# Kernel tuning notes

Hardware: AMD Instinct MI355X
Metric: run time of the kernel (lower is better)

Reference implementation:

```python
import jax, jax.numpy as jnp
import numpy as np

X_DIM, Y_DIM = 16, 8
D_MODEL, N_HEADS, N_LAYERS = 256, 8, 8
D_HEAD = D_MODEL // N_HEADS            # 32 (hidden_out_size // n_heads)
D_FF = D_HEAD * 8 * N_HEADS            # 2048 (feed_forward_dimensions)
B, S_PAST, S_FUT = 4, 1024, 512
MIN_STD = 0.01
LN_EPS = 1e-5
ATTN_EPS = 1e-6


def setup_inputs() -> dict:
    key = jax.random.key(0)
    ks = jax.random.split(key, 24)
    def nrm(k, shape, s=0.02):
        return jax.random.normal(k, shape, jnp.float32) * s
    L, d, dff = N_LAYERS, D_MODEL, D_FF
    x_size = X_DIM + Y_DIM
    return {
        "past_x": jax.random.normal(ks[0], (B, S_PAST, X_DIM), jnp.float32),
        "past_y": jax.random.normal(ks[1], (B, S_PAST, Y_DIM), jnp.float32),
        "future_x": jax.random.normal(ks[2], (B, S_FUT, X_DIM), jnp.float32),
        "enc_W": nrm(ks[3], (x_size, d)), "enc_b": jnp.zeros((d,), jnp.float32),
        "Wq": nrm(ks[4], (L, d, d)), "bq": jnp.zeros((L, d), jnp.float32),
        "Wk": nrm(ks[5], (L, d, d)), "bk": jnp.zeros((L, d), jnp.float32),
        "Wv": nrm(ks[6], (L, d, d)), "bv": jnp.zeros((L, d), jnp.float32),
        "Wo": nrm(ks[7], (L, d, d)), "bo": jnp.zeros((L, d), jnp.float32),
        "ln1_w": jnp.ones((L, d), jnp.float32), "ln1_b": jnp.zeros((L, d), jnp.float32),
        "W1": nrm(ks[8], (L, d, dff)), "b1": jnp.zeros((L, dff), jnp.float32),
        "W2": nrm(ks[9], (L, dff, d)), "b2": jnp.zeros((L, d), jnp.float32),
        "ln2_w": jnp.ones((L, d), jnp.float32), "ln2_b": jnp.zeros((L, d), jnp.float32),
        "mean_W": nrm(ks[10], (d, Y_DIM)), "mean_b": jnp.zeros((Y_DIM,), jnp.float32),
        "std_W": nrm(ks[11], (d, Y_DIM)), "std_b": jnp.zeros((Y_DIM,), jnp.float32),
    }


def _ln(x, w, b):
    m = jnp.mean(x, axis=-1, keepdims=True)
    v = jnp.var(x, axis=-1, keepdims=True)
    return (x - m) * jax.lax.rsqrt(v + LN_EPS) * w + b


def _causal_linear_attn(q, k, v):
    # q,k,v: [B, N, H, D]; phi(x) = elu(x) + 1 (fast_transformers default feature map)
    q = jax.nn.elu(q) + 1.0
    k = jax.nn.elu(k) + 1.0
    # cumulative outer-product state S_i = sum_{j<=i} phi(k_j) v_j^T : [B,N,H,D,D]
    kv = jnp.cumsum(jnp.einsum('bnhd,bnhm->bnhdm', k, v), axis=1)
    num = jnp.einsum('bnhd,bnhdm->bnhm', q, kv)
    z = jnp.einsum('bnhd,bnhd->bnh', q, jnp.cumsum(k, axis=1))
    return num / (z[..., None] + ATTN_EPS)


def _forward(past_x, past_y, future_x, enc_W, enc_b, Wq, bq, Wk, bk, Wv, bv,
             Wo, bo, ln1_w, ln1_b, W1, b1, W2, b2, ln2_w, ln2_b,
             mean_W, mean_b, std_W, std_b):
    Bz, Sf = future_x.shape[0], future_x.shape[1]
    steps = past_y.shape[1]
    # future y placeholder = last observed y, repeated
    fy = jnp.repeat(past_y[:, -1:, :], Sf, axis=1)
    context = jnp.concatenate([past_x, past_y], axis=-1)
    target = jnp.concatenate([future_x, fy], axis=-1)
    x = jax.lax.stop_gradient(jnp.concatenate([context, target], axis=1))  # .detach()
    x = x @ enc_W + enc_b                      # [B, N, D_MODEL]
    N = x.shape[1]
    for i in range(N_LAYERS):
        q = (x @ Wq[i] + bq[i]).reshape(Bz, N, N_HEADS, D_HEAD)
        k = (x @ Wk[i] + bk[i]).reshape(Bz, N, N_HEADS, D_HEAD)
        v = (x @ Wv[i] + bv[i]).reshape(Bz, N, N_HEADS, D_HEAD)
        a = _causal_linear_attn(q, k, v).reshape(Bz, N, D_MODEL)
        x = _ln(x + (a @ Wo[i] + bo[i]), ln1_w[i], ln1_b[i])   # post-norm (fast_transformers)
        y = jax.nn.relu(x @ W1[i] + b1[i]) @ W2[i] + b2[i]
        x = _ln(x + y, ln2_w[i], ln2_b[i])
    out = x[:, steps:, :]                      # keep only the target segment
    mean = out @ mean_W + mean_b
    sigma = MIN_STD + (1.0 - MIN_STD) * jax.nn.softplus(out @ std_W + std_b)
    return mean, sigma


def reference(past_x, past_y, future_x, enc_W, enc_b, Wq, bq, Wk, bk, Wv, bv,
              Wo, bo, ln1_w, ln1_b, W1, b1, W2, b2, ln2_w, ln2_b,
              mean_W, mean_b, std_W, std_b):
    return _forward(past_x, past_y, future_x, enc_W, enc_b, Wq, bq, Wk, bk,
                    Wv, bv, Wo, bo, ln1_w, ln1_b, W1, b1, W2, b2,
                    ln2_w, ln2_b, mean_W, mean_b, std_W, std_b)
```

## Files before the change

### kernel.cpp

```cpp
#include <hip/hip_runtime.h>
#include <hip/hip_bf16.h>
#include <math.h>

#define BB 4
#define SP 1024
#define SF 512
#define NN 1536
#define DD 256
#define HH 8
#define DH 32
#define DFF 2048
#define LL 8
#define TOK (BB*NN)
#define FTOK (BB*SF)
#define NSEG 48
#define SEGLEN 32

typedef __attribute__((ext_vector_type(8))) short bf16x8;
typedef __attribute__((ext_vector_type(4))) float f32x4;
typedef __hip_bfloat16 bf16;

__device__ __forceinline__ void gld_lds16(const void* g, void* l) {
    __builtin_amdgcn_global_load_lds(
        (const __attribute__((address_space(1))) void*)g,
        (__attribute__((address_space(3))) void*)l, 16, 0, 0);
}

__device__ __forceinline__ unsigned short f2bf_u(float f) {
    return __builtin_bit_cast(unsigned short, __float2bfloat16(f));
}

__device__ __forceinline__ int futmap(int f) {
    return (f >> 9)*NN + SP + (f & 511);
}

__device__ __forceinline__ void wtrans_tile(
    const float* __restrict__ s, bf16* __restrict__ d, int K, int N,
    int k0, int n0)
{
    __shared__ float tile[64][65];
    int t = threadIdx.x, c = t & 63, r4 = t >> 6;
    #pragma unroll
    for (int rr = 0; rr < 64; rr += 4)
        tile[rr+r4][c] = s[(size_t)(k0+rr+r4)*N + n0 + c];
    __syncthreads();
    #pragma unroll
    for (int rr = 0; rr < 64; rr += 4) {
        int n = rr + r4;
        d[(size_t)(n0+n)*K + k0 + c] = __float2bfloat16(tile[c][n]);
    }
}

__global__ __launch_bounds__(256) void wtrans_kernel(
    const float* __restrict__ src, bf16* __restrict__ dst, int K, int N)
{
    wtrans_tile(src + (size_t)blockIdx.z*K*N, dst + (size_t)blockIdx.z*K*N,
                K, N, blockIdx.x*64, blockIdx.y*64);
}

__global__ __launch_bounds__(256) void wtrans4_kernel(
    const float* __restrict__ Wq, const float* __restrict__ Wk,
    const float* __restrict__ Wv, const float* __restrict__ Wo,
    bf16* __restrict__ Wqt, bf16* __restrict__ Wkt,
    bf16* __restrict__ Wvt, bf16* __restrict__ Wot)
{
    int z = blockIdx.z, which = z >> 3, l = z & 7;
    const float* s = (which == 0 ? Wq : which == 1 ? Wk : which == 2 ? Wv : Wo)
                     + (size_t)l*DD*DD;
    bf16* d = (which == 0 ? Wqt : which == 1 ? Wkt : which == 2 ? Wvt : Wot)
              + (size_t)l*DD*DD;
    wtrans_tile(s, d, DD, DD, blockIdx.x*64, blockIdx.y*64);
}

template<int BM, bool BOUT>
__device__ __forceinline__ void gemm_core(
    const bf16* __restrict__ A, const bf16* __restrict__ Wt,
    const float* __restrict__ bias, float* __restrict__ Cf,
    bf16* __restrict__ Cb, int N, int K, int epi, int kc0, int kc1, int fut)
{
    constexpr int MI = BM/32;
    __shared__ bf16 As[BM*64];
    __shared__ bf16 Bs[128*64];
    int tid = threadIdx.x, lane = tid & 63, wid = tid >> 6;
    int m0 = blockIdx.x*BM, n0 = blockIdx.y*128;
    if (fut) m0 = futmap(m0);
    int wm = (wid & 1)*(BM/2), wn = (wid >> 1)*64;

    f32x4 acc[MI][4] = {};

    int rA = wid*(BM/4) + (lane >> 3);
    int rB = wid*32 + (lane >> 3);
    int c_st = (lane & 7)*8;
    const bf16* Ag = A  + (size_t)(m0 + rA)*K + c_st;
    const bf16* Bg = Wt + (size_t)(n0 + rB)*K + c_st;
    bf16* Asw = As + (wid*(BM/4))*64;
    bf16* Bsw = Bs + (wid*32)*64;

    int a_off = (wm + (lane & 15))*64 + (lane >> 4)*8;
    int b_off = (wn + (lane & 15))*64 + (lane >> 4)*8;

    for (int kc = kc0; kc < kc1; kc += 64) {
        #pragma unroll
        for (int i = 0; i < MI; i++)
            gld_lds16(Ag + (size_t)(i*8)*K + kc, Asw + (i*8)*64);
        #pragma unroll
        for (int i = 0; i < 4; i++)
            gld_lds16(Bg + (size_t)(i*8)*K + kc, Bsw + (i*8)*64);
        __syncthreads();
        #pragma unroll
        for (int ks = 0; ks < 2; ks++) {
            bf16x8 af[MI], bfr[4];
            #pragma unroll
            for (int i = 0; i < MI; i++)
                af[i] = *(const bf16x8*)(As + a_off + i*16*64 + ks*32);
            #pragma unroll
            for (int j = 0; j < 4; j++)
                bfr[j] = *(const bf16x8*)(Bs + b_off + j*16*64 + ks*32);
            #pragma unroll
            for (int i = 0; i < MI; i++)
                #pragma unroll
                for (int j = 0; j < 4; j++)
                    acc[i][j] = __builtin_amdgcn_mfma_f32_16x16x32_bf16(
                        af[i], bfr[j], acc[i][j], 0, 0, 0);
        }
        __syncthreads();
    }

    if constexpr (BOUT) {
        bf16* Ct = Bs;
        #pragma unroll
        for (int j = 0; j < 4; j++) {
            int col = wn + j*16 + (lane & 15);
            float bv = bias[n0 + col];
            #pragma unroll
            for (int i = 0; i < MI; i++) {
                #pragma unroll
                for (int r = 0; r < 4; r++) {
                    int row = wm + i*16 + (lane >> 4)*4 + r;
                    float v = acc[i][j][r] + bv;
                    if (epi == 1) v = fmaxf(v, 0.f);
                    else if (epi == 2) v = (v > 0.f) ? v + 1.f : expf(v);
                    Ct[row*128 + (col ^ (((row >> 2) & 3) << 4))] = __float2bfloat16(v);
                }
            }
        }
        __syncthreads();
        constexpr int NU = BM/16;
        #pragma unroll
        for (int u = 0; u < NU; u++) {
            int e = (u*256 + tid)*8;
            int row = e >> 7, c0 = e & 127;
            bf16x8 val = *(const bf16x8*)(Ct + row*128 + (c0 ^ (((row >> 2) & 3) << 4)));
            *(bf16x8*)(Cb + (size_t)(m0 + row)*N + n0 + c0) = val;
        }
    } else {
        int col_base = n0 + wn + (lane & 15);
        int row_base = m0 + wm + (lane >> 4)*4;
        #pragma unroll
        for (int j = 0; j < 4; j++) {
            int col = col_base + j*16;
            float bv = bias[col];
            #pragma unroll
            for (int i = 0; i < MI; i++) {
                #pragma unroll
                for (int r = 0; r < 4; r++) {
                    int row = row_base + i*16 + r;
                    float v = acc[i][j][r] + bv;
                    if (epi == 1) v = fmaxf(v, 0.f);
                    else if (epi == 2) v = (v > 0.f) ? v + 1.f : expf(v);
                    if (Cb) Cb[(size_t)row*N + col] = __float2bfloat16(v);
                    else    Cf[(size_t)row*N + col] = v;
                }
            }
        }
    }
}

template<int BM, bool BOUT>
__global__ __launch_bounds__(256) void mfma_gemm_kernel(
    const bf16* __restrict__ A, const bf16* __restrict__ Wt,
    const float* __restrict__ bias, float* __restrict__ Cf,
    bf16* __restrict__ Cb, int N, int K, int epi, int fut)
{
    gemm_core<BM, BOUT>(A, Wt, bias, Cf, Cb, N, K, epi, 0, K, fut);
}

template<int BM>
__global__ __launch_bounds__(256) void mfma_qkv_kernel(
    const bf16* __restrict__ Xb,
    const bf16* __restrict__ Wqt, const bf16* __restrict__ Wkt, const bf16* __restrict__ Wvt,
    const float* __restrict__ bq, const float* __restrict__ bk, const float* __restrict__ bv,
    float* __restrict__ Q, float* __restrict__ K, float* __restrict__ V, int layer)
{
    int z = blockIdx.z;
    const bf16* Wt = (z == 0) ? Wqt : (z == 1) ? Wkt : Wvt;
    const float* b = (z == 0) ? bq : (z == 1) ? bk : bv;
    float* C = (z == 0) ? Q : (z == 1) ? K : V;
    gemm_core<BM, false>(Xb, Wt + (size_t)layer*DD*DD, b + (size_t)layer*DD,
                         C, nullptr, DD, DD, (z == 2) ? 0 : 2, 0, DD, 0);
}

__global__ __launch_bounds__(256) void w2_slice_kernel(
    const bf16* __restrict__ A, const bf16* __restrict__ Wt,
    float* __restrict__ G4, int fut)
{
    __shared__ bf16 As[32*64];
    __shared__ bf16 Bs[256*64];
    int tid = threadIdx.x, lane = tid & 63, wid = tid >> 6;
    int m0 = blockIdx.x*32;
    if (fut) m0 = futmap(m0);
    int z = blockIdx.y;
    int kc0 = z*(DFF/4), kc1 = kc0 + DFF/4;
    int wn = wid*64;

    f32x4 acc[2][4] = {};

    int rA = wid*8 + (lane >> 3);
    int c_st = (lane & 7)*8;
    const bf16* Ag = A + (size_t)(m0 + rA)*DFF + c_st;
    const bf16* Bg = Wt + (size_t)(wn + (lane >> 3))*DFF + c_st;
    bf16* Asw = As + (wid*8)*64;
    bf16* Bsw = Bs + wn*64;

    int a_off = (lane & 15)*64 + (lane >> 4)*8;
    int b_off = (wn + (lane & 15))*64 + (lane >> 4)*8;

    for (int kc = kc0; kc < kc1; kc += 64) {
        gld_lds16(Ag + kc, Asw);
        #pragma unroll
        for (int i = 0; i < 8; i++)
            gld_lds16(Bg + (size_t)(i*8)*DFF + kc, Bsw + (i*8)*64);
        __syncthreads();
        #pragma unroll
        for (int ks = 0; ks < 2; ks++) {
            bf16x8 af[2], bfr[4];
            af[0] = *(const bf16x8*)(As + a_off + ks*32);
            af[1] = *(const bf16x8*)(As + a_off + 16*64 + ks*32);
            #pragma unroll
            for (int j = 0; j < 4; j++)
                bfr[j] = *(const bf16x8*)(Bs + b_off + j*16*64 + ks*32);
            #pragma unroll
            for (int i = 0; i < 2; i++)
                #pragma unroll
                for (int j = 0; j < 4; j++)
                    acc[i][j] = __builtin_amdgcn_mfma_f32_16x16x32_bf16(
                        af[i], bfr[j], acc[i][j], 0, 0, 0);
        }
        __syncthreads();
    }

    float* Gz = G4 + (size_t)z*TOK*DD;
    #pragma unroll
    for (int j = 0; j < 4; j++) {
        int c = wn + j*16 + (lane & 15);
        #pragma unroll
        for (int i = 0; i < 2; i++) {
            int row = m0 + i*16 + (lane >> 4)*4;
            #pragma unroll
            for (int r = 0; r < 4; r++)
                Gz[(size_t)(row + r)*DD + c] = acc[i][j][r];
        }
    }
}

__global__ __launch_bounds__(256) void wo_ln_kernel(
    const bf16* __restrict__ A, const bf16* __restrict__ Wt,
    const float* __restrict__ bias,
    const float* __restrict__ lnw, const float* __restrict__ lnb,
    float* __restrict__ X, bf16* __restrict__ Xb, int fut)
{
    __shared__ bf16 As[32*64];
    __shared__ bf16 Bs[256*64];
    __shared__ float red[2][4][32];
    int tid = threadIdx.x, lane = tid & 63, wid = tid >> 6;
    int m0 = blockIdx.x*32;
    if (fut) m0 = futmap(m0);
    int wn = wid*64;

    f32x4 acc[2][4] = {};

    int rA = wid*8 + (lane >> 3);
    int c_st = (lane & 7)*8;
    const bf16* Ag = A + (size_t)(m0 + rA)*DD + c_st;
    const bf16* Bg = Wt + (size_t)(wn + (lane >> 3))*DD + c_st;
    bf16* Asw = As + (wid*8)*64;
    bf16* Bsw = Bs + wn*64;

    int a_off = (lane & 15)*64 + (lane >> 4)*8;
    int b_off = (wn + (lane & 15))*64 + (lane >> 4)*8;

    for (int kc = 0; kc < DD; kc += 64) {
        gld_lds16(Ag + kc, Asw);
        #pragma unroll
        for (int i = 0; i < 8; i++)
            gld_lds16(Bg + (size_t)(i*8)*DD + kc, Bsw + (i*8)*64);
        __syncthreads();
        #pragma unroll
        for (int ks = 0; ks < 2; ks++) {
            bf16x8 af[2], bfr[4];
            af[0] = *(const bf16x8*)(As + a_off + ks*32);
            af[1] = *(const bf16x8*)(As + a_off + 16*64 + ks*32);
            #pragma unroll
            for (int j = 0; j < 4; j++)
                bfr[j] = *(const bf16x8*)(Bs + b_off + j*16*64 + ks*32);
            #pragma unroll
            for (int i = 0; i < 2; i++)
                #pragma unroll
                for (int j = 0; j < 4; j++)
                    acc[i][j] = __builtin_amdgcn_mfma_f32_16x16x32_bf16(
                        af[i], bfr[j], acc[i][j], 0, 0, 0);
        }
        __syncthreads();
    }

    #pragma unroll
    for (int j = 0; j < 4; j++) {
        int c = wn + j*16 + (lane & 15);
        float bv = bias[c];
        #pragma unroll
        for (int i = 0; i < 2; i++) {
            int row = m0 + i*16 + (lane >> 4)*4;
            #pragma unroll
            for (int r = 0; r < 4; r++)
                acc[i][j][r] += bv + X[(size_t)(row + r)*DD + c];
        }
    }
    #pragma unroll
    for (int i = 0; i < 2; i++) {
        #pragma unroll
        for (int r = 0; r < 4; r++) {
            float s  = (acc[i][0][r] + acc[i][1][r]) + (acc[i][2][r] + acc[i][3][r]);
            float s2 = (acc[i][0][r]*acc[i][0][r] + acc[i][1][r]*acc[i][1][r])
                     + (acc[i][2][r]*acc[i][2][r] + acc[i][3][r]*acc[i][3][r]);
            #pragma unroll
            for (int off = 1; off < 16; off <<= 1) {
                s  += __shfl_xor(s,  off, 64);
                s2 += __shfl_xor(s2, off, 64);
            }
            if ((lane & 15) == 0) {
                int rloc = i*16 + (lane >> 4)*4 + r;
                red[0][wid][rloc] = s;
                red[1][wid][rloc] = s2;
            }
        }
    }
    __syncthreads();
    #pragma unroll
    for (int i = 0; i < 2; i++) {
        #pragma unroll
        for (int r = 0; r < 4; r++) {
            int rloc = i*16 + (lane >> 4)*4 + r;
            float S  = (red[0][0][rloc] + red[0][1][rloc]) + (red[0][2][rloc] + red[0][3][rloc]);
            float S2 = (red[1][0][rloc] + red[1][1][rloc]) + (red[1][2][rloc] + red[1][3][rloc]);
            float mean = S * (1.f/256.f);
            float var  = S2 * (1.f/256.f) - mean*mean;
            float rs = rsqrtf(var + 1e-5f);
            #pragma unroll
            for (int j = 0; j < 4; j++) {
                int c = wn + j*16 + (lane & 15);
                float o = (acc[i][j][r] - mean) * rs * lnw[c] + lnb[c];
                size_t idx = (size_t)(m0 + rloc)*DD + c;
                X[idx] = o;
                Xb[idx] = __float2bfloat16(o);
            }
        }
    }
}

__global__ __launch_bounds__(256) void encode_kernel(
    const float* __restrict__ px, const float* __restrict__ py,
    const float* __restrict__ fx, const float* __restrict__ encW,
    const float* __restrict__ encb, float* __restrict__ X, bf16* __restrict__ Xb)
{
    int tok = blockIdx.x;
    int t = threadIdx.x;
    int b = tok / NN, n = tok % NN;
    __shared__ float in[24];
    if (t < 16) {
        in[t] = (n < SP) ? px[((size_t)b*SP + n)*16 + t]
                         : fx[((size_t)b*SF + (n - SP))*16 + t];
    } else if (t < 24) {
        int j = t - 16;
        in[t] = (n < SP) ? py[((size_t)b*SP + n)*8 + j]
                         : py[((size_t)b*SP + (SP-1))*8 + j];
    }
    __syncthreads();
    float acc = encb[t];
    #pragma unroll
    for (int j = 0; j < 24; j++) acc = fmaf(in[j], encW[j*DD + t], acc);
    X[(size_t)tok*DD + t] = acc;
    Xb[(size_t)tok*DD + t] = __float2bfloat16(acc);
}

__global__ __launch_bounds__(256) void attnA_kernel(
    const float* __restrict__ K, const float* __restrict__ V,
    float* __restrict__ SegS, float* __restrict__ SegZ)
{
    int bid = blockIdx.x;
    int seg = bid % NSEG; int bh = bid / NSEG;
    int h = bh & 7, b = bh >> 3;
    int t = threadIdx.x;
    int d = t & 31, mg = t >> 5, m0 = mg*4;
    int tok0 = b*NN + seg*SEGLEN;
    const float* Kp = K + (size_t)tok0*DD + h*DH;
    const float* Vp = V + (size_t)tok0*DD + h*DH;
    float a0=0,a1=0,a2=0,a3=0, ks=0;
    #pragma unroll 4
    for (int i = 0; i < SEGLEN; i++) {
        float kd = Kp[(size_t)i*DD + d];
        float4 vv = *(const float4*)(Vp + (size_t)i*DD + m0);
        a0 = fmaf(kd, vv.x, a0); a1 = fmaf(kd, vv.y, a1);
        a2 = fmaf(kd, vv.z, a2); a3 = fmaf(kd, vv.w, a3);
        ks += kd;
    }
    float4 o = {a0, a1, a2, a3};
    *(float4*)(SegS + ((size_t)bid*32 + d)*32 + m0) = o;
    if (mg == 0) SegZ[(size_t)bid*32 + d] = ks;
}

__global__ __launch_bounds__(256) void attnA2_kernel(
    float* __restrict__ SegS, float* __restrict__ SegZ)
{
    int bh = blockIdx.x, y = blockIdx.y, t = threadIdx.x;
    int e = y*256 + t;
    float* p = SegS + (size_t)bh*NSEG*1024 + e;
    float v[NSEG];
    #pragma unroll
    for (int s = 0; s < NSEG; s++) v[s] = p[(size_t)s*1024];
    float run = 0.f;
    #pragma unroll
    for (int s = 0; s < NSEG; s++) {
        p[(size_t)s*1024] = run;
        run += v[s];
    }
    if (y == 0 && t < 32) {
        float* pz = SegZ + (size_t)bh*NSEG*32 + t;
        float vz[NSEG];
        #pragma unroll
        for (int s = 0; s < NSEG; s++) vz[s] = pz[(size_t)s*32];
        float runz = 0.f;
        #pragma unroll
        for (int s = 0; s < NSEG; s++) {
            pz[(size_t)s*32] = runz;
            runz += vz[s];
        }
    }
}

__global__ __launch_bounds__(256) void attnB_kernel(
    const float* __restrict__ Q, const float* __restrict__ K, const float* __restrict__ V,
    const float* __restrict__ SegS, const float* __restrict__ SegZ,
    bf16* __restrict__ A, int seg0, int nsegl)
{
    int tid = threadIdx.x;
    int sidx = tid >> 7;
    int half = (tid >> 6) & 1;
    int lane = tid & 63;
    int lbid = blockIdx.x*2 + sidx;
    int seg = seg0 + lbid % nsegl;
    int bh = lbid / nsegl;
    int gbid = bh*NSEG + seg;
    int h = bh & 7, b = bh >> 3;
    int m = half*16 + (lane & 15);
    int d0 = (lane >> 4)*8;
    int tok0 = b*NN + seg*SEGLEN;

    __shared__ float qs[2][SEGLEN][32], ksm[2][SEGLEN][32], vs[2][SEGLEN][32];
    const float* Qp = Q + (size_t)tok0*DD + h*DH;
    const float* Kp = K + (size_t)tok0*DD + h*DH;
    const float* Vp = V + (size_t)tok0*DD + h*DH;
    int lt = tid & 127;
    #pragma unroll
    for (int f = lt; f < SEGLEN*8; f += 128) {
        int r = f >> 3, c = (f & 7)*4;
        *(float4*)&qs[sidx][r][c]  = *(const float4*)(Qp + (size_t)r*DD + c);
        *(float4*)&ksm[sidx][r][c] = *(const float4*)(Kp + (size_t)r*DD + c);
        *(float4*)&vs[sidx][r][c]  = *(const float4*)(Vp + (size_t)r*DD + c);
    }
    __syncthreads();

    float kv[8], kss[8];
    const float* Pp = SegS + (size_t)gbid*1024;
    const float* Zp = SegZ + (size_t)gbid*32;
    #pragma unroll
    for (int j = 0; j < 8; j++) {
        kv[j]  = Pp[(d0 + j)*32 + m];
        kss[j] = Zp[d0 + j];
    }

    bf16* Ap = A + (size_t)tok0*DD + h*DH;
    for (int i = 0; i < SEGLEN; i++) {
        float qv[8], kk[8];
        #pragma unroll
        for (int c = 0; c < 2; c++) {
            float4 t4 = *(const float4*)&qs[sidx][i][d0 + 4*c];
            qv[4*c] = t4.x; qv[4*c+1] = t4.y; qv[4*c+2] = t4.z; qv[4*c+3] = t4.w;
            float4 k4 = *(const float4*)&ksm[sidx][i][d0 + 4*c];
            kk[4*c] = k4.x; kk[4*c+1] = k4.y; kk[4*c+2] = k4.z; kk[4*c+3] = k4.w;
        }
        float vm = vs[sidx][i][m];
        #pragma unroll
        for (int j = 0; j < 8; j++) {
            kv[j] = fmaf(kk[j], vm, kv[j]);
            kss[j] += kk[j];
        }
        float p0=0,p1=0,z0=0,z1=0;
        #pragma unroll
        for (int j = 0; j < 4; j++) {
            p0 = fmaf(qv[j],   kv[j],   p0);
            p1 = fmaf(qv[4+j], kv[4+j], p1);
            z0 = fmaf(qv[j],   kss[j],  z0);
            z1 = fmaf(qv[4+j], kss[4+j],z1);
        }
        float nump = p0 + p1;
        float zp   = z0 + z1;
        nump += __shfl_xor(nump, 16, 64);
        nump += __shfl_xor(nump, 32, 64);
        zp   += __shfl_xor(zp,   16, 64);
        zp   += __shfl_xor(zp,   32, 64);
        if ((lane >> 4) == 0)
            Ap[(size_t)i*DD + m] = __float2bfloat16(nump / (zp + 1e-6f));
    }
}

__global__ __launch_bounds__(256) void resid_ln4_kernel(
    const float* __restrict__ Xin, const float* __restrict__ G4,
    const float* __restrict__ gb,
    const float* __restrict__ w, const float* __restrict__ b,
    float* __restrict__ Xout, bf16* __restrict__ Xbout, int fut)
{
    const size_t SZ = (size_t)TOK*DD;
    int tok = blockIdx.x, t = threadIdx.x;
    if (fut) tok = futmap(tok);
    size_t idx = (size_t)tok*DD + t;
    float v = Xin[idx] + gb[t]
            + ((G4[idx] + G4[SZ + idx]) + (G4[2*SZ + idx] + G4[3*SZ + idx]));
    float s = v, s2 = v*v;
    #pragma unroll
    for (int off = 32; off >= 1; off >>= 1) {
        s  += __shfl_xor(s,  off, 64);
        s2 += __shfl_xor(s2, off, 64);
    }
    __shared__ float ps[4], ps2[4];
    int wid = t >> 6;
    if ((t & 63) == 0) { ps[wid] = s; ps2[wid] = s2; }
    __syncthreads();
    float S  = ps[0] + ps[1] + ps[2] + ps[3];
    float S2 = ps2[0] + ps2[1] + ps2[2] + ps2[3];
    float mean = S * (1.f/256.f);
    float var  = S2 * (1.f/256.f) - mean*mean;
    float o = (v - mean) * rsqrtf(var + 1e-5f) * w[t] + b[t];
    Xout[idx] = o;
    Xbout[idx] = __float2bfloat16(o);
}

__global__ __launch_bounds__(256) void head_kernel(
    const float* __restrict__ X,
    const float* __restrict__ meanW, const float* __restrict__ meanB,
    const float* __restrict__ stdW,  const float* __restrict__ stdB,
    float* __restrict__ out)
{
    int wv = threadIdx.x >> 6;
    int lane = threadIdx.x & 63;
    int idx = blockIdx.x*4 + wv;
    int b = idx / SF, i = idx % SF;
    const float* row = X + ((size_t)(b*NN + SP + i))*DD;
    __shared__ float xs[4][DD];
    *(float4*)&xs[wv][lane*4] = *(const float4*)(row + lane*4);
    __syncthreads();

    int j = lane & 7;
    int which = (lane >> 3) & 1;
    int seg = lane >> 4;
    const float* W = which ? stdW : meanW;
    float p = 0.f;
    #pragma unroll 16
    for (int d = seg*64; d < seg*64 + 64; d++) p = fmaf(xs[wv][d], W[d*8 + j], p);
    p += __shfl_xor(p, 16, 64);
    p += __shfl_xor(p, 32, 64);
    if (lane < 16) {
        if (which == 0) {
            out[((size_t)b*SF + i)*8 + j] = p + meanB[j];
        } else {
            float s = p + stdB[j];
            float sp = fmaxf(s, 0.f) + log1pf(expf(-fabsf(s)));
            out[(size_t)BB*SF*8 + ((size_t)b*SF + i)*8 + j] = 0.01f + 0.99f*sp;
        }
    }
}

extern "C" void kernel_launch(void* const* d_in, const int* in_sizes, int n_in,
                              void* d_out, int out_size, void* d_ws, size_t ws_size,
                              hipStream_t stream)
{
    (void)in_sizes; (void)n_in; (void)out_size; (void)ws_size;
    const float* past_x   = (const float*)d_in[0];
    const float* past_y   = (const float*)d_in[1];
    const float* future_x = (const float*)d_in[2];
    const float* enc_W    = (const float*)d_in[3];
    const float* enc_b    = (const float*)d_in[4];
    const float* Wq       = (const float*)d_in[5];
    const float* bq       = (const float*)d_in[6];
    const float* Wk       = (const float*)d_in[7];
    const float* bk       = (const float*)d_in[8];
    const float* Wv       = (const float*)d_in[9];
    const float* bv       = (const float*)d_in[10];
    const float* Wo       = (const float*)d_in[11];
    const float* bo       = (const float*)d_in[12];
    const float* ln1_w    = (const float*)d_in[13];
    const float* ln1_b    = (const float*)d_in[14];
    const float* W1       = (const float*)d_in[15];
    const float* b1       = (const float*)d_in[16];
    const float* W2       = (const float*)d_in[17];
    const float* b2       = (const float*)d_in[18];
    const float* ln2_w    = (const float*)d_in[19];
    const float* ln2_b    = (const float*)d_in[20];
    const float* mean_W   = (const float*)d_in[21];
    const float* mean_b   = (const float*)d_in[22];
    const float* std_W    = (const float*)d_in[23];
    const float* std_b    = (const float*)d_in[24];
    float* out = (float*)d_out;

    char* base = (char*)d_ws;
    size_t off = 0;
    float* X  = (float*)(base + off); off += (size_t)TOK*DD*4;
    bf16* Xb  = (bf16*)(base + off);  off += (size_t)TOK*DD*2;
    bf16* Hb  = (bf16*)(base + off);  off += (size_t)TOK*DFF*2;
    float* Qb = (float*)Hb;
    float* Kb = Qb + (size_t)TOK*DD;
    float* Vb = Kb + (size_t)TOK*DD;
    bf16* Ab  = (bf16*)(base + off);  off += (size_t)TOK*DD*2;
    float* G4 = (float*)(base + off); off += (size_t)4*TOK*DD*4;
    float* SegS = (float*)(base + off); off += (size_t)BB*HH*NSEG*1024*4;
    float* SegZ = (float*)(base + off); off += (size_t)BB*HH*NSEG*32*4;
    bf16* Wqt = (bf16*)(base + off); off += (size_t)LL*DD*DD*2;
    bf16* Wkt = (bf16*)(base + off); off += (size_t)LL*DD*DD*2;
    bf16* Wvt = (bf16*)(base + off); off += (size_t)LL*DD*DD*2;
    bf16* Wot = (bf16*)(base + off); off += (size_t)LL*DD*DD*2;
    bf16* W1t = (bf16*)(base + off); off += (size_t)LL*DD*DFF*2;
    bf16* W2t = (bf16*)(base + off); off += (size_t)LL*DFF*DD*2;

    wtrans4_kernel<<<dim3(4, 4, 4*LL), 256, 0, stream>>>(
        Wq, Wk, Wv, Wo, Wqt, Wkt, Wvt, Wot);
    wtrans_kernel<<<dim3(4, 32, LL), 256, 0, stream>>>(W1, W1t, DD, DFF);
    wtrans_kernel<<<dim3(32, 4, LL), 256, 0, stream>>>(W2, W2t, DFF, DD);

    encode_kernel<<<TOK, 256, 0, stream>>>(past_x, past_y, future_x, enc_W, enc_b, X, Xb);

    for (int l = 0; l < LL; l++) {
        int last = (l == LL - 1);
        mfma_qkv_kernel<32><<<dim3(TOK/32, 2, 3), 256, 0, stream>>>(
            Xb, Wqt, Wkt, Wvt, bq, bk, bv, Qb, Kb, Vb, l);
        attnA_kernel<<<BB*HH*NSEG, 256, 0, stream>>>(Kb, Vb, SegS, SegZ);
        attnA2_kernel<<<dim3(BB*HH, 4), 256, 0, stream>>>(SegS, SegZ);
        if (!last) {
            attnB_kernel<<<BB*HH*NSEG/2, 256, 0, stream>>>(
                Qb, Kb, Vb, SegS, SegZ, Ab, 0, NSEG);
            wo_ln_kernel<<<TOK/32, 256, 0, stream>>>(
                Ab, Wot + (size_t)l*DD*DD, bo + (size_t)l*DD,
                ln1_w + l*DD, ln1_b + l*DD, X, Xb, 0);
            mfma_gemm_kernel<32, true><<<dim3(TOK/32, DFF/128), 256, 0, stream>>>(
                Xb, W1t + (size_t)l*DD*DFF, b1 + (size_t)l*DFF, nullptr, Hb, DFF, DD, 1, 0);
            w2_slice_kernel<<<dim3(TOK/32, 4), 256, 0, stream>>>(
                Hb, W2t + (size_t)l*DFF*DD, G4, 0);
            resid_ln4_kernel<<<TOK, 256, 0, stream>>>(
                X, G4, b2 + (size_t)l*DD, ln2_w + l*DD, ln2_b + l*DD, X, Xb, 0);
        } else {
            attnB_kernel<<<BB*HH*16/2, 256, 0, stream>>>(
                Qb, Kb, Vb, SegS, SegZ, Ab, 32, 16);
            wo_ln_kernel<<<FTOK/32, 256, 0, stream>>>(
                Ab, Wot + (size_t)l*DD*DD, bo + (size_t)l*DD,
                ln1_w + l*DD, ln1_b + l*DD, X, Xb, 1);
            mfma_gemm_kernel<32, true><<<dim3(FTOK/32, DFF/128), 256, 0, stream>>>(
                Xb, W1t + (size_t)l*DD*DFF, b1 + (size_t)l*DFF, nullptr, Hb, DFF, DD, 1, 1);
            w2_slice_kernel<<<dim3(FTOK/32, 4), 256, 0, stream>>>(
                Hb, W2t + (size_t)l*DFF*DD, G4, 1);
            resid_ln4_kernel<<<FTOK, 256, 0, stream>>>(
                X, G4, b2 + (size_t)l*DD, ln2_w + l*DD, ln2_b + l*DD, X, Xb, 1);
        }
    }

    head_kernel<<<(BB*SF)/4, 256, 0, stream>>>(X, mean_W, mean_b, std_W, std_b, out);
}
```

Baseline: 945.3 us.

## Fold segment prefix scan into attnB and drop attnA2 kernel

```diff
diff --git a/kernel.cpp b/kernel.cpp
--- a/kernel.cpp
+++ b/kernel.cpp
@@ -400,50 +400,25 @@
     int seg = bid % NSEG; int bh = bid / NSEG;
     int h = bh & 7, b = bh >> 3;
     int t = threadIdx.x;
-    int d = t & 31, mg = t >> 5, m0 = mg*4;
+    int m = t & 31, dg = t >> 5, d0 = dg*4;
     int tok0 = b*NN + seg*SEGLEN;
     const float* Kp = K + (size_t)tok0*DD + h*DH;
     const float* Vp = V + (size_t)tok0*DD + h*DH;
-    float a0=0,a1=0,a2=0,a3=0, ks=0;
+    float a0=0,a1=0,a2=0,a3=0;
+    float k0s=0,k1s=0,k2s=0,k3s=0;
     #pragma unroll 4
     for (int i = 0; i < SEGLEN; i++) {
-        float kd = Kp[(size_t)i*DD + d];
-        float4 vv = *(const float4*)(Vp + (size_t)i*DD + m0);
-        a0 = fmaf(kd, vv.x, a0); a1 = fmaf(kd, vv.y, a1);
-        a2 = fmaf(kd, vv.z, a2); a3 = fmaf(kd, vv.w, a3);
-        ks += kd;
+        float4 kk = *(const float4*)(Kp + (size_t)i*DD + d0);
+        float vm = Vp[(size_t)i*DD + m];
+        a0 = fmaf(kk.x, vm, a0); a1 = fmaf(kk.y, vm, a1);
+        a2 = fmaf(kk.z, vm, a2); a3 = fmaf(kk.w, vm, a3);
+        k0s += kk.x; k1s += kk.y; k2s += kk.z; k3s += kk.w;
     }
     float4 o = {a0, a1, a2, a3};
-    *(float4*)(SegS + ((size_t)bid*32 + d)*32 + m0) = o;
-    if (mg == 0) SegZ[(size_t)bid*32 + d] = ks;
-}
-
-__global__ __launch_bounds__(256) void attnA2_kernel(
-    float* __restrict__ SegS, float* __restrict__ SegZ)
-{
-    int bh = blockIdx.x, y = blockIdx.y, t = threadIdx.x;
-    int e = y*256 + t;
-    float* p = SegS + (size_t)bh*NSEG*1024 + e;
-    float v[NSEG];
-    #pragma unroll
-    for (int s = 0; s < NSEG; s++) v[s] = p[(size_t)s*1024];
-    float run = 0.f;
-    #pragma unroll
-    for (int s = 0; s < NSEG; s++) {
-        p[(size_t)s*1024] = run;
-        run += v[s];
-    }
-    if (y == 0 && t < 32) {
-        float* pz = SegZ + (size_t)bh*NSEG*32 + t;
-        float vz[NSEG];
-        #pragma unroll
-        for (int s = 0; s < NSEG; s++) vz[s] = pz[(size_t)s*32];
-        float runz = 0.f;
-        #pragma unroll
-        for (int s = 0; s < NSEG; s++) {
-            pz[(size_t)s*32] = runz;
-            runz += vz[s];
-        }
+    *(float4*)(SegS + ((size_t)bid*32 + m)*32 + d0) = o;
+    if (m == 0) {
+        float4 kz = {k0s, k1s, k2s, k3s};
+        *(float4*)(SegZ + (size_t)bid*32 + d0) = kz;
     }
 }
 
@@ -459,7 +434,6 @@
     int lbid = blockIdx.x*2 + sidx;
     int seg = seg0 + lbid % nsegl;
     int bh = lbid / nsegl;
-    int gbid = bh*NSEG + seg;
     int h = bh & 7, b = bh >> 3;
     int m = half*16 + (lane & 15);
     int d0 = (lane >> 4)*8;
@@ -479,13 +453,18 @@
     }
     __syncthreads();
 
-    float kv[8], kss[8];
-    const float* Pp = SegS + (size_t)gbid*1024;
-    const float* Zp = SegZ + (size_t)gbid*32;
-    #pragma unroll
-    for (int j = 0; j < 8; j++) {
-        kv[j]  = Pp[(d0 + j)*32 + m];
-        kss[j] = Zp[d0 + j];
+    float kv[8] = {0,0,0,0,0,0,0,0}, kss[8] = {0,0,0,0,0,0,0,0};
+    const float* PpB = SegS + (size_t)(bh*NSEG)*1024 + m*32 + d0;
+    const float* ZpB = SegZ + (size_t)(bh*NSEG)*32 + d0;
+    for (int s = 0; s < seg; s++) {
+        float4 p0 = *(const float4*)(PpB + (size_t)s*1024);
+        float4 p1 = *(const float4*)(PpB + (size_t)s*1024 + 4);
+        float4 z0 = *(const float4*)(ZpB + (size_t)s*32);
+        float4 z1 = *(const float4*)(ZpB + (size_t)s*32 + 4);
+        kv[0] += p0.x; kv[1] += p0.y; kv[2] += p0.z; kv[3] += p0.w;
+        kv[4] += p1.x; kv[5] += p1.y; kv[6] += p1.z; kv[7] += p1.w;
+        kss[0] += z0.x; kss[1] += z0.y; kss[2] += z0.z; kss[3] += z0.w;
+        kss[4] += z1.x; kss[5] += z1.y; kss[6] += z1.z; kss[7] += z1.w;
     }
 
     bf16* Ap = A + (size_t)tok0*DD + h*DH;
@@ -652,7 +631,6 @@
         mfma_qkv_kernel<32><<<dim3(TOK/32, 2, 3), 256, 0, stream>>>(
             Xb, Wqt, Wkt, Wvt, bq, bk, bv, Qb, Kb, Vb, l);
         attnA_kernel<<<BB*HH*NSEG, 256, 0, stream>>>(Kb, Vb, SegS, SegZ);
-        attnA2_kernel<<<dim3(BB*HH, 4), 256, 0, stream>>>(SegS, SegZ);
         if (!last) {
             attnB_kernel<<<BB*HH*NSEG/2, 256, 0, stream>>>(
                 Qb, Kb, Vb, SegS, SegZ, Ab, 0, NSEG);
```

Result: slower. 1.069 ms (+13.1%).
